# Performance work log

Hardware: AMD Instinct MI355X
Metric: run time of the kernel (lower is better)

The kernel has to match this reference:

```python
import jax, jax.numpy as jnp
import numpy as np

GROUPSIZE = 128
# 6 possible 2:4 sparsity patterns (choose 2 nonzeros out of each group of 4 rows)
_PATTERNS = jnp.array([
    [1, 1, 0, 0], [1, 0, 1, 0], [1, 0, 0, 1],
    [0, 1, 1, 0], [0, 1, 0, 1], [0, 0, 1, 1],
], dtype=jnp.float32)


def setup_inputs() -> dict:
    key = jax.random.key(0)
    k1, k2, k3, k4 = jax.random.split(key, 4)
    M, K, N = 4096, 4096, 8192
    x = jax.random.normal(k1, (M, K), dtype=jnp.float16)
    # int4 codes in [0, 15] (stored unpacked; bit-packing is layout-only)
    qweight = jax.random.randint(k2, (K, N), 0, 16, dtype=jnp.int32)
    # 2:4 pattern index per group of 4 consecutive K rows
    meta = jax.random.randint(k3, (K // 4, N), 0, 6, dtype=jnp.int32)
    # positive group scales, typical quantization magnitude
    scale = (jax.random.uniform(k4, (K // GROUPSIZE, N), dtype=jnp.float32) * 0.02 + 0.005).astype(jnp.float16)
    return {"x": x, "qweight": qweweight_fix(qweight), "meta": meta, "scale": scale}


def qweweight_fix(q):
    return q  # identity; kept for clarity


def _dequant(qweight, meta, scale):
    """Dequantize int4 2:4-sparse weights with group scales -> dense fp32 [K, N]."""
    K, N = qweight.shape
    mask = _PATTERNS[meta]                      # [K//4, N, 4]
    mask = jnp.transpose(mask, (0, 2, 1)).reshape(K, N)  # [K, N]
    s = jnp.repeat(scale.astype(jnp.float32), GROUPSIZE, axis=0)  # [K, N]
    # symmetric int4: zero-point = 8 (maxq+1)//2
    return (qweight.astype(jnp.float32) - 8.0) * mask * s


def reference(x, qweight, meta, scale):
    W = _dequant(qweight, meta, scale)          # [K, N] fp32
    out = x.astype(jnp.float32) @ W             # fp32 accumulation, as in the kernel
    return out.astype(x.dtype)                  # [M, N] fp16
```

## Files before the change

kernel.cpp:

```cpp
#include <hip/hip_runtime.h>
#include <cmath>


typedef __attribute__((ext_vector_type(8))) short bf16x8;
typedef __attribute__((ext_vector_type(4))) float f32x4;

__device__ inline unsigned short f2bf(float f) {
    union { float f; unsigned u; } v; v.f = f;
    unsigned r = (v.u + 0x7FFFu + ((v.u >> 16) & 1u)) >> 16;
    return (unsigned short)r;
}

__global__ __launch_bounds__(256) void convert_x(
    const float* __restrict__ x, unsigned short* __restrict__ xb, long long total)
{
    const long long base = ((long long)blockIdx.x * 256 + threadIdx.x) * 8;
    if (base + 8 > total) return;
    const float4 a = *reinterpret_cast<const float4*>(x + base);
    const float4 b = *reinterpret_cast<const float4*>(x + base + 4);
    uint4 o;
    o.x = (unsigned)f2bf(a.x) | ((unsigned)f2bf(a.y) << 16);
    o.y = (unsigned)f2bf(a.z) | ((unsigned)f2bf(a.w) << 16);
    o.z = (unsigned)f2bf(b.x) | ((unsigned)f2bf(b.y) << 16);
    o.w = (unsigned)f2bf(b.z) | ((unsigned)f2bf(b.w) << 16);
    *reinterpret_cast<uint4*>(xb + base) = o;
}

__global__ __launch_bounds__(256) void dequant_wt(
    const int* __restrict__ q, const int* __restrict__ meta,
    const float* __restrict__ scale,
    unsigned short* __restrict__ wt,
    int K, int N, int nbase)
{
    __shared__ __align__(16) unsigned short lds[64 * 68];
    const int t  = threadIdx.x;
    const int n  = t & 63;
    const int kc = t >> 6;
    const int k0 = blockIdx.x * 64;
    const int nl0 = blockIdx.y * 64;
    const int ng = nbase + nl0 + n;
    const int g = k0 >> 7;
    const float sc = scale[(size_t)g * N + ng];
    const unsigned lut = 0xCA6953u;

    #pragma unroll
    for (int p = 0; p < 4; ++p) {
        const int kl = p * 16 + kc * 4;
        const int kg = k0 + kl;
        const int mv = meta[(size_t)(kg >> 2) * N + ng];
        const unsigned pat = (lut >> (mv * 4)) & 0xFu;
        unsigned short w[4];
        #pragma unroll
        for (int j = 0; j < 4; ++j) {
            const int qv = q[(size_t)(kg + j) * N + ng];
            const float wf = ((pat >> j) & 1u) ? (float)(qv - 8) * sc : 0.0f;
            w[j] = f2bf(wf);
        }
        uint2 pk;
        pk.x = (unsigned)w[0] | ((unsigned)w[1] << 16);
        pk.y = (unsigned)w[2] | ((unsigned)w[3] << 16);
        *reinterpret_cast<uint2*>(&lds[n * 68 + kl]) = pk;
    }
    __syncthreads();
    #pragma unroll
    for (int p = 0; p < 2; ++p) {
        const int idx = p * 256 + t;
        const int nr  = idx >> 3;
        const int ch  = idx & 7;
        const uint2 lo = *reinterpret_cast<const uint2*>(&lds[nr * 68 + ch * 8]);
        const uint2 hi = *reinterpret_cast<const uint2*>(&lds[nr * 68 + ch * 8 + 4]);
        uint4 vv; vv.x = lo.x; vv.y = lo.y; vv.z = hi.x; vv.w = hi.y;
        *reinterpret_cast<uint4*>(&wt[(size_t)(nl0 + nr) * K + k0 + ch * 8]) = vv;
    }
}

#define BAR() do { asm volatile("" ::: "memory"); \
                   __builtin_amdgcn_s_barrier(); \
                   asm volatile("" ::: "memory"); } while (0)

#define GLDS(g, s) __builtin_amdgcn_global_load_lds( \
    (const __attribute__((address_space(1))) void*)(g), \
    (__attribute__((address_space(3))) void*)(s), 16, 0, 0)

#define MFMA(d, x, y) d = __builtin_amdgcn_mfma_f32_16x16x32_bf16(x, y, d, 0, 0, 0)

__global__ __launch_bounds__(512, 2) void gemm256(
    const unsigned short* __restrict__ A,
    const unsigned short* __restrict__ Bt,
    float* __restrict__ C,
    int M, int N, int K, int nbase)
{
    __shared__ __align__(16) unsigned short As[32768];
    __shared__ __align__(16) unsigned short Bs[32768];

    const int t    = threadIdx.x;
    const int w    = t >> 6;
    const int lane = t & 63;
    const int wm   = w >> 2;
    const int wn   = w & 3;
    const int l16  = lane & 15;
    const int quad = lane >> 4;

    const int gx = gridDim.x, gy = gridDim.y;
    int bid = blockIdx.y * gx + blockIdx.x;
    const int nwg = gx * gy;
    int m0, n0;
    if ((nwg & 7) == 0 && (gy & 1) == 0 && (gx & 3) == 0) {
        const int xcd = bid & 7;
        const int idx = bid >> 3;
        const int cpr = gx >> 2;
        const int lr  = idx / cpr;
        const int lc  = idx - lr * cpr;
        m0 = ((xcd >> 2) * (gy >> 1) + lr) * 256;
        n0 = ((xcd & 3) * cpr + lc) * 256;
    } else {
        int b2 = bid;
        if (nwg >= 8) {
            const int q8 = nwg >> 3, r8 = nwg & 7;
            const int xcd = bid & 7, off = bid >> 3;
            b2 = (xcd < r8 ? xcd * (q8 + 1) : r8 * (q8 + 1) + (xcd - r8) * q8) + off;
        }
        n0 = (b2 % gx) * 256;
        m0 = (b2 / gx) * 256;
    }

    const int    csrc = ((lane & 7) ^ ((lane >> 3) & 7)) * 8;
    const size_t aB = (size_t)(m0 + w * 8 + (lane >> 3)) * K + csrc;
    const size_t bB = (size_t)(n0 + w * 8 + (lane >> 3)) * K + csrc;
    const size_t J  = (size_t)64 * K;
    const size_t H  = (size_t)128 * K;
    const int sdst  = w * 512;

    const int sw0 = ((quad ^ (lane & 7)) * 8);
    const int sw1 = (((4 + quad) ^ (lane & 7)) * 8);
    const int aR  = wm * 8192 + l16 * 64;
    const int bR  = (wn >> 1) * 8192 + ((wn & 1) * 64 + l16) * 64;

    int kA = 0, kB = 0;

#define STAGE_A(buf, h) do { \
    GLDS(A + aB + (size_t)(h) * H + kA, &As[(buf)*16384 + (h)*8192 + sdst]); \
    GLDS(A + aB + (size_t)(h) * H + J + kA, &As[(buf)*16384 + (h)*8192 + 4096 + sdst]); \
  } while (0)
#define STAGE_B(buf, h) do { \
    GLDS(Bt + bB + (size_t)(h) * H + kB, &Bs[(buf)*16384 + (h)*8192 + sdst]); \
    GLDS(Bt + bB + (size_t)(h) * H + J + kB, &Bs[(buf)*16384 + (h)*8192 + 4096 + sdst]); \
  } while (0)

    f32x4 acc[8][4];
    #pragma unroll
    for (int i = 0; i < 8; ++i)
        #pragma unroll
        for (int j = 0; j < 4; ++j)
            acc[i][j] = (f32x4){0.f, 0.f, 0.f, 0.f};

    STAGE_B(0, 0); STAGE_B(0, 1); kB += 64;
    STAGE_A(0, 0); STAGE_A(0, 1); kA += 64;
    STAGE_B(1, 0); STAGE_B(1, 1); kB += 64;
    asm volatile("s_waitcnt vmcnt(4)" ::: "memory");
    BAR();

    bf16x8 a[4][2], bA_[2][2], bB_[2][2];

    #pragma unroll
    for (int j = 0; j < 2; ++j) {
        bA_[j][0] = *(const bf16x8*)&Bs[bR + j * 1024 + sw0];
        bA_[j][1] = *(const bf16x8*)&Bs[bR + j * 1024 + sw1];
    }

#define PHASES(buf, obuf, bcur, bnxt) do { \
   \
  _Pragma("unroll") for (int i = 0; i < 4; ++i) { \
    a[i][0] = *(const bf16x8*)&As[(buf)*16384 + aR + i*1024 + sw0]; \
    a[i][1] = *(const bf16x8*)&As[(buf)*16384 + aR + i*1024 + sw1]; } \
  STAGE_A(obuf, 0); STAGE_A(obuf, 1); kA += 64; if (kA >= K) kA = 0; \
  BAR(); \
  asm volatile("s_waitcnt lgkmcnt(0)" ::: "memory"); \
  __builtin_amdgcn_s_setprio(1); \
  _Pragma("unroll") for (int i = 0; i < 4; ++i) \
    _Pragma("unroll") for (int j = 0; j < 2; ++j) { \
      MFMA(acc[i][j], a[i][0], bcur[j][0]); MFMA(acc[i][j], a[i][1], bcur[j][1]); } \
  __builtin_amdgcn_s_setprio(0); \
  BAR(); \
   \
  _Pragma("unroll") for (int j = 0; j < 2; ++j) { \
    bnxt[j][0] = *(const bf16x8*)&Bs[(buf)*16384 + bR + (2+j)*1024 + sw0]; \
    bnxt[j][1] = *(const bf16x8*)&Bs[(buf)*16384 + bR + (2+j)*1024 + sw1]; } \
  BAR(); \
  asm volatile("s_waitcnt lgkmcnt(0)" ::: "memory"); \
  __builtin_amdgcn_s_setprio(1); \
  _Pragma("unroll") for (int i = 0; i < 4; ++i) \
    _Pragma("unroll") for (int j = 0; j < 2; ++j) { \
      MFMA(acc[i][2+j], a[i][0], bnxt[j][0]); MFMA(acc[i][2+j], a[i][1], bnxt[j][1]); } \
  __builtin_amdgcn_s_setprio(0); \
  BAR(); \
   \
  _Pragma("unroll") for (int i = 0; i < 4; ++i) { \
    a[i][0] = *(const bf16x8*)&As[(buf)*16384 + aR + (4+i)*1024 + sw0]; \
    a[i][1] = *(const bf16x8*)&As[(buf)*16384 + aR + (4+i)*1024 + sw1]; } \
  STAGE_B(buf, 0); \
  BAR(); \
  asm volatile("s_waitcnt lgkmcnt(0)" ::: "memory"); \
  __builtin_amdgcn_s_setprio(1); \
  _Pragma("unroll") for (int i = 0; i < 4; ++i) \
    _Pragma("unroll") for (int j = 0; j < 2; ++j) { \
      MFMA(acc[4+i][2+j], a[i][0], bnxt[j][0]); MFMA(acc[4+i][2+j], a[i][1], bnxt[j][1]); } \
  __builtin_amdgcn_s_setprio(0); \
  BAR(); \
   \
   \
  asm volatile("s_waitcnt vmcnt(6)" ::: "memory"); \
  _Pragma("unroll") for (int j = 0; j < 2; ++j) { \
    bnxt[j][0] = *(const bf16x8*)&Bs[(obuf)*16384 + bR + j*1024 + sw0]; \
    bnxt[j][1] = *(const bf16x8*)&Bs[(obuf)*16384 + bR + j*1024 + sw1]; } \
  STAGE_B(buf, 1); kB += 64; if (kB >= K) kB = 0; \
  BAR(); \
  asm volatile("s_waitcnt lgkmcnt(0)" ::: "memory"); \
  __builtin_amdgcn_s_setprio(1); \
  _Pragma("unroll") for (int i = 0; i < 4; ++i) \
    _Pragma("unroll") for (int j = 0; j < 2; ++j) { \
      MFMA(acc[4+i][j], a[i][0], bcur[j][0]); MFMA(acc[4+i][j], a[i][1], bcur[j][1]); } \
  __builtin_amdgcn_s_setprio(0); \
  asm volatile("s_waitcnt vmcnt(4)" ::: "memory"); \
  BAR(); \
} while (0)

    const int NIT = K >> 7;
    for (int it = 0; it < NIT; ++it) {
        PHASES(0, 1, bA_, bB_);
        PHASES(1, 0, bB_, bA_);
    }

    asm volatile("s_waitcnt vmcnt(0)" ::: "memory");

    const int mBase = m0 + wm * 128;
    const int nBase = nbase + n0 + wn * 64;
    #pragma unroll
    for (int i = 0; i < 8; ++i) {
        const int mrow = mBase + i * 16 + quad * 4;
        #pragma unroll
        for (int j = 0; j < 4; ++j) {
            const int ncol = nBase + j * 16 + l16;
            #pragma unroll
            for (int r = 0; r < 4; ++r)
                C[(size_t)(mrow + r) * N + ncol] = acc[i][j][r];
        }
    }
#undef STAGE_A
#undef STAGE_B
#undef PHASES
}

extern "C" void kernel_launch(void* const* d_in, const int* in_sizes, int n_in,
                              void* d_out, int out_size, void* d_ws, size_t ws_size,
                              hipStream_t stream)
{
    const float* x     = (const float*)d_in[0];
    const int*   q     = (const int*)d_in[1];
    const int*   meta  = (const int*)d_in[2];
    const float* scale = (const float*)d_in[3];
    float*       out   = (float*)d_out;

    const double s0 = (double)in_sizes[0];
    const double s1 = (double)in_sizes[1];
    const int K = (int)llround(sqrt(s0 * s1 / (double)out_size));
    const int M = in_sizes[0] / K;
    const int N = in_sizes[1] / K;

    unsigned short* xb = (unsigned short*)d_ws;
    const size_t xb_bytes = (size_t)M * (size_t)K * 2;
    unsigned short* wt = (unsigned short*)((char*)d_ws + xb_bytes);
    const size_t wt_avail = ws_size > xb_bytes ? ws_size - xb_bytes : 0;

    const long long total = (long long)M * K;
    convert_x<<<dim3((unsigned)((total / 8 + 255) / 256)), dim3(256), 0, stream>>>(
        x, xb, total);

    long long maxrows = (long long)(wt_avail / ((size_t)K * 2));
    int NC = (int)((maxrows / 256) * 256);
    if (NC > N) NC = N;
    if (NC < 256) NC = 256;

    for (int nbase = 0; nbase < N; nbase += NC) {
        const int nc = (N - nbase) < NC ? (N - nbase) : NC;
        dim3 g1(K / 64, nc / 64);
        dequant_wt<<<g1, dim3(256), 0, stream>>>(q, meta, scale, wt, K, N, nbase);
        dim3 g2(nc / 256, M / 256);
        gemm256<<<g2, dim3(512), 0, stream>>>(xb, wt, out, M, N, K, nbase);
    }
}
```

Baseline: 560.9 us.

## Fuse x conversion into dequant kernel, swizzle LDS, split GEMM launch by M halves

```diff
diff --git a/kernel.cpp b/kernel.cpp
--- a/kernel.cpp
+++ b/kernel.cpp
@@ -11,55 +11,60 @@
     return (unsigned short)r;
 }
 
-__global__ __launch_bounds__(256) void convert_x(
-    const float* __restrict__ x, unsigned short* __restrict__ xb, long long total)
-{
-    const long long base = ((long long)blockIdx.x * 256 + threadIdx.x) * 8;
-    if (base + 8 > total) return;
-    const float4 a = *reinterpret_cast<const float4*>(x + base);
-    const float4 b = *reinterpret_cast<const float4*>(x + base + 4);
-    uint4 o;
-    o.x = (unsigned)f2bf(a.x) | ((unsigned)f2bf(a.y) << 16);
-    o.y = (unsigned)f2bf(a.z) | ((unsigned)f2bf(a.w) << 16);
-    o.z = (unsigned)f2bf(b.x) | ((unsigned)f2bf(b.y) << 16);
-    o.w = (unsigned)f2bf(b.z) | ((unsigned)f2bf(b.w) << 16);
-    *reinterpret_cast<uint4*>(xb + base) = o;
-}
-
-__global__ __launch_bounds__(256) void dequant_wt(
+__global__ __launch_bounds__(256) void dequant_conv(
     const int* __restrict__ q, const int* __restrict__ meta,
     const float* __restrict__ scale,
     unsigned short* __restrict__ wt,
+    const float* __restrict__ x, unsigned short* __restrict__ xb,
+    long long total, int gyD,
     int K, int N, int nbase)
 {
-    __shared__ __align__(16) unsigned short lds[64 * 68];
-    const int t  = threadIdx.x;
-    const int n  = t & 63;
-    const int kc = t >> 6;
-    const int k0 = blockIdx.x * 64;
-    const int nl0 = blockIdx.y * 64;
-    const int ng = nbase + nl0 + n;
-    const int g = k0 >> 7;
-    const float sc = scale[(size_t)g * N + ng];
+    __shared__ __align__(16) unsigned short lds[64 * 64];
+    const int t = threadIdx.x;
+
+    if ((int)blockIdx.y >= gyD) {
+        const long long cid = (long long)((int)blockIdx.y - gyD) * gridDim.x
+                            + blockIdx.x;
+        const long long base = (cid * 256 + t) * 8;
+        if (base + 8 > total) return;
+        const float4 a = *reinterpret_cast<const float4*>(x + base);
+        const float4 b = *reinterpret_cast<const float4*>(x + base + 4);
+        uint4 o;
+        o.x = (unsigned)f2bf(a.x) | ((unsigned)f2bf(a.y) << 16);
+        o.y = (unsigned)f2bf(a.z) | ((unsigned)f2bf(a.w) << 16);
+        o.z = (unsigned)f2bf(b.x) | ((unsigned)f2bf(b.y) << 16);
+        o.w = (unsigned)f2bf(b.z) | ((unsigned)f2bf(b.w) << 16);
+        *reinterpret_cast<uint4*>(xb + base) = o;
+        return;
+    }
+
+    const int nlane = t & 15;
+    const int kc    = t >> 4;
+    const int k0    = blockIdx.x * 64;
+    const int nl0   = blockIdx.y * 64;
+    const int g     = k0 >> 7;
+    const int kbase = k0 + kc * 4;
     const unsigned lut = 0xCA6953u;
 
     #pragma unroll
-    for (int p = 0; p < 4; ++p) {
-        const int kl = p * 16 + kc * 4;
-        const int kg = k0 + kl;
-        const int mv = meta[(size_t)(kg >> 2) * N + ng];
+    for (int nn = 0; nn < 4; ++nn) {
+        const int r  = nlane + nn * 16;
+        const int ng = nbase + nl0 + r;
+        const float sc = scale[(size_t)g * N + ng];
+        const int mv = meta[(size_t)(kbase >> 2) * N + ng];
         const unsigned pat = (lut >> (mv * 4)) & 0xFu;
         unsigned short w[4];
         #pragma unroll
         for (int j = 0; j < 4; ++j) {
-            const int qv = q[(size_t)(kg + j) * N + ng];
+            const int qv = q[(size_t)(kbase + j) * N + ng];
             const float wf = ((pat >> j) & 1u) ? (float)(qv - 8) * sc : 0.0f;
             w[j] = f2bf(wf);
         }
         uint2 pk;
         pk.x = (unsigned)w[0] | ((unsigned)w[1] << 16);
         pk.y = (unsigned)w[2] | ((unsigned)w[3] << 16);
-        *reinterpret_cast<uint2*>(&lds[n * 68 + kl]) = pk;
+        const int off = r * 64 + ((((kc >> 1) ^ (r & 7)) << 3) | ((kc & 1) << 2));
+        *reinterpret_cast<uint2*>(&lds[off]) = pk;
     }
     __syncthreads();
     #pragma unroll
@@ -67,9 +72,8 @@
         const int idx = p * 256 + t;
         const int nr  = idx >> 3;
         const int ch  = idx & 7;
-        const uint2 lo = *reinterpret_cast<const uint2*>(&lds[nr * 68 + ch * 8]);
-        const uint2 hi = *reinterpret_cast<const uint2*>(&lds[nr * 68 + ch * 8 + 4]);
-        uint4 vv; vv.x = lo.x; vv.y = lo.y; vv.z = hi.x; vv.w = hi.y;
+        const uint4 vv = *reinterpret_cast<const uint4*>(
+            &lds[nr * 64 + ((ch ^ (nr & 7)) << 3)]);
         *reinterpret_cast<uint4*>(&wt[(size_t)(nl0 + nr) * K + k0 + ch * 8]) = vv;
     }
 }
@@ -88,7 +92,7 @@
     const unsigned short* __restrict__ A,
     const unsigned short* __restrict__ Bt,
     float* __restrict__ C,
-    int M, int N, int K, int nbase)
+    int M, int N, int K, int nbase, int mbase)
 {
     __shared__ __align__(16) unsigned short As[32768];
     __shared__ __align__(16) unsigned short Bs[32768];
@@ -123,6 +127,7 @@
         n0 = (b2 % gx) * 256;
         m0 = (b2 / gx) * 256;
     }
+    m0 += mbase;
 
     const int    csrc = ((lane & 7) ^ ((lane >> 3) & 7)) * 8;
     const size_t aB = (size_t)(m0 + w * 8 + (lane >> 3)) * K + csrc;
@@ -154,8 +159,8 @@
         for (int j = 0; j < 4; ++j)
             acc[i][j] = (f32x4){0.f, 0.f, 0.f, 0.f};
 
+    STAGE_A(0, 0); STAGE_A(0, 1); kA += 64;
     STAGE_B(0, 0); STAGE_B(0, 1); kB += 64;
-    STAGE_A(0, 0); STAGE_A(0, 1); kA += 64;
     STAGE_B(1, 0); STAGE_B(1, 1); kB += 64;
     asm volatile("s_waitcnt vmcnt(4)" ::: "memory");
     BAR();
@@ -169,11 +174,10 @@
     }
 
 #define PHASES(buf, obuf, bcur, bnxt) do { \
-   \
   _Pragma("unroll") for (int i = 0; i < 4; ++i) { \
     a[i][0] = *(const bf16x8*)&As[(buf)*16384 + aR + i*1024 + sw0]; \
     a[i][1] = *(const bf16x8*)&As[(buf)*16384 + aR + i*1024 + sw1]; } \
-  STAGE_A(obuf, 0); STAGE_A(obuf, 1); kA += 64; if (kA >= K) kA = 0; \
+  STAGE_A(obuf, 0); \
   BAR(); \
   asm volatile("s_waitcnt lgkmcnt(0)" ::: "memory"); \
   __builtin_amdgcn_s_setprio(1); \
@@ -182,10 +186,10 @@
       MFMA(acc[i][j], a[i][0], bcur[j][0]); MFMA(acc[i][j], a[i][1], bcur[j][1]); } \
   __builtin_amdgcn_s_setprio(0); \
   BAR(); \
-   \
   _Pragma("unroll") for (int j = 0; j < 2; ++j) { \
     bnxt[j][0] = *(const bf16x8*)&Bs[(buf)*16384 + bR + (2+j)*1024 + sw0]; \
     bnxt[j][1] = *(const bf16x8*)&Bs[(buf)*16384 + bR + (2+j)*1024 + sw1]; } \
+  STAGE_A(obuf, 1); kA += 64; if (kA >= K) kA = 0; \
   BAR(); \
   asm volatile("s_waitcnt lgkmcnt(0)" ::: "memory"); \
   __builtin_amdgcn_s_setprio(1); \
@@ -194,7 +198,6 @@
       MFMA(acc[i][2+j], a[i][0], bnxt[j][0]); MFMA(acc[i][2+j], a[i][1], bnxt[j][1]); } \
   __builtin_amdgcn_s_setprio(0); \
   BAR(); \
-   \
   _Pragma("unroll") for (int i = 0; i < 4; ++i) { \
     a[i][0] = *(const bf16x8*)&As[(buf)*16384 + aR + (4+i)*1024 + sw0]; \
     a[i][1] = *(const bf16x8*)&As[(buf)*16384 + aR + (4+i)*1024 + sw1]; } \
@@ -206,10 +209,8 @@
     _Pragma("unroll") for (int j = 0; j < 2; ++j) { \
       MFMA(acc[4+i][2+j], a[i][0], bnxt[j][0]); MFMA(acc[4+i][2+j], a[i][1], bnxt[j][1]); } \
   __builtin_amdgcn_s_setprio(0); \
-  BAR(); \
-   \
-   \
   asm volatile("s_waitcnt vmcnt(6)" ::: "memory"); \
+  BAR(); \
   _Pragma("unroll") for (int j = 0; j < 2; ++j) { \
     bnxt[j][0] = *(const bf16x8*)&Bs[(obuf)*16384 + bR + j*1024 + sw0]; \
     bnxt[j][1] = *(const bf16x8*)&Bs[(obuf)*16384 + bR + j*1024 + sw1]; } \
@@ -273,19 +274,27 @@
     const size_t wt_avail = ws_size > xb_bytes ? ws_size - xb_bytes : 0;
 
     const long long total = (long long)M * K;
-    convert_x<<<dim3((unsigned)((total / 8 + 255) / 256)), dim3(256), 0, stream>>>(
-        x, xb, total);
-
     long long maxrows = (long long)(wt_avail / ((size_t)K * 2));
     int NC = (int)((maxrows / 256) * 256);
     if (NC > N) NC = N;
     if (NC < 256) NC = 256;
 
+    const int gxD = K / 64;
+    const long long conv_blocks = (total / 8 + 255) / 256;
+
     for (int nbase = 0; nbase < N; nbase += NC) {
         const int nc = (N - nbase) < NC ? (N - nbase) : NC;
-        dim3 g1(K / 64, nc / 64);
-        dequant_wt<<<g1, dim3(256), 0, stream>>>(q, meta, scale, wt, K, N, nbase);
-        dim3 g2(nc / 256, M / 256);
-        gemm256<<<g2, dim3(512), 0, stream>>>(xb, wt, out, M, N, K, nbase);
+        const int gyD = nc / 64;
+        const int gyC = (nbase == 0)
+            ? (int)((conv_blocks + gxD - 1) / gxD) : 0;
+        dim3 g1(gxD, gyD + gyC);
+        dequant_conv<<<g1, dim3(256), 0, stream>>>(
+            q, meta, scale, wt, x, xb, total, gyD, K, N, nbase);
+        const int Mh = M / 2;
+        for (int h = 0; h < 2; ++h) {
+            dim3 g2(nc / 256, Mh / 256);
+            gemm256<<<g2, dim3(512), 0, stream>>>(
+                xb, wt, out, M, N, K, nbase, h * Mh);
+        }
     }
 }
```

Result: no change. 566.9 us (+1.1%).
